# Kernel tuning notes

Hardware: AMD Instinct MI355X
Metric: run time of the kernel (lower is better)

Reference implementation:

```python
import jax, jax.numpy as jnp
from jax import lax
import numpy as np

B, R, NOBJ = 16, 64, 36
MAP = 64

def setup_inputs() -> dict:
    key = jax.random.key(0)
    ks = jax.random.split(key, 8)
    W, H = 1280, 720
    xs = jnp.sort(jax.random.uniform(ks[0], (B, NOBJ, 2), minval=0.0, maxval=float(W)), axis=-1)
    ys = jnp.sort(jax.random.uniform(ks[1], (B, NOBJ, 2), minval=0.0, maxval=float(H)), axis=-1)
    # bbox layout: [x0, y0, x1, y1] matching scale_bbox (x scaled by width, y by height)
    bboxes = jnp.stack([xs[..., 0], ys[..., 0], xs[..., 1], ys[..., 1]], axis=-1)
    obj_pairs = jax.random.randint(ks[2], (B, R, 2), 0, NOBJ, dtype=jnp.int32)
    num_rels = jnp.full((B,), R, dtype=jnp.int32)
    W1 = jax.random.normal(ks[3], (64, 2, 5, 5), jnp.float32) * 0.1
    b1 = jnp.zeros((64,), jnp.float32)
    W2 = jax.random.normal(ks[4], (32, 64, 5, 5), jnp.float32) * 0.05
    b2 = jnp.zeros((32,), jnp.float32)
    Wl = jax.random.normal(ks[5], (32, 512), jnp.float32) * 0.1
    bl = jnp.zeros((512,), jnp.float32)
    return {"bboxes": bboxes, "obj_pairs": obj_pairs, "num_rels": num_rels,
            "frame_width": W, "frame_height": H,
            "W1": W1, "b1": b1, "W2": W2, "b2": b2, "Wl": Wl, "bl": bl}

def _boxes_to_maps(boxes, frame_width, frame_height):
    # boxes: [T,4] = [x0,y0,x1,y1]; emulate scale_bbox + int() truncation + slice fill
    sfx = MAP / frame_width
    sfy = MAP / frame_height
    x0 = jnp.floor(boxes[:, 0] * sfx).astype(jnp.int32)  # col start
    x1 = jnp.floor(boxes[:, 2] * sfx).astype(jnp.int32)  # col end (exclusive)
    y0 = jnp.floor(boxes[:, 1] * sfy).astype(jnp.int32)  # row start
    y1 = jnp.floor(boxes[:, 3] * sfy).astype(jnp.int32)  # row end (exclusive)
    ix = jnp.arange(MAP)
    rows = (ix[None, :] >= y0[:, None]) & (ix[None, :] < y1[:, None])  # [T,64]
    cols = (ix[None, :] >= x0[:, None]) & (ix[None, :] < x1[:, None])  # [T,64]
    return (rows[:, :, None] & cols[:, None, :]).astype(jnp.float32)   # [T,64,64]

def _conv(x, W, b):
    y = lax.conv_general_dilated(x, W, (1, 1), 'VALID',
                                 dimension_numbers=('NCHW', 'OIHW', 'NCHW'))
    return y + b[None, :, None, None]

def _maxpool2(x):
    return lax.reduce_window(x, -jnp.inf, lax.max, (1, 1, 2, 2), (1, 1, 2, 2), 'VALID')

def reference(bboxes, obj_pairs, num_rels, frame_width, frame_height,
              W1, b1, W2, b2, Wl, bl):
    Bn = bboxes.shape[0]
    bi = jnp.arange(Bn)[:, None]
    box_a = bboxes[bi, obj_pairs[..., 0]].reshape(-1, 4)  # [T,4]
    box_b = bboxes[bi, obj_pairs[..., 1]].reshape(-1, 4)  # [T,4]
    sp = jnp.stack([_boxes_to_maps(box_a, frame_width, frame_height),
                    _boxes_to_maps(box_b, frame_width, frame_height)], axis=1)  # [T,2,64,64]
    x = _maxpool2(_conv(sp, W1, b1))        # [T,64,30,30]
    x = _maxpool2(_conv(x, W2, b2))         # [T,32,13,13]
    x = jnp.mean(x, axis=(2, 3))            # AvgPool 13x13 stride 1 -> [T,32]
    return jax.nn.relu(x @ Wl + bl)         # [T,512]
```

## Files before the change

kernel.cpp:

```cpp
#include <hip/hip_runtime.h>
#include <hip/hip_bf16.h>

#define BLOCK 1024
#define NREG  21

typedef __attribute__((ext_vector_type(8))) short short8;
typedef __attribute__((ext_vector_type(4))) float floatx4;
typedef __attribute__((ext_vector_type(4))) unsigned int uint4v;

#define SMEM_Q     0
#define SMEM_POOL  0
#define SMEM_P     72064
#define SMEM_V     72064
#define SMEM_FEAT  135568
#define SMEM_INFO  135696
#define SMEM_REP   135936
#define SMEM_TOTAL 136192

__device__ __forceinline__ int clamp05(int v) { return v < 0 ? 0 : (v > 5 ? 5 : v); }

__device__ __forceinline__ int band_id(int i, int e0, int e1, int e2, int e3) {
    int c = 0;
    #pragma unroll
    for (int k = 0; k < 5; ++k) {
        const int b0 = e0 - k, b1 = e1 - k, b2 = e2 - k, b3 = e3 - k;
        c += (b0 >= 1 && i >= b0);
        c += (b1 >= 1 && i >= b1);
        c += (b2 >= 1 && i >= b2);
        c += (b3 >= 1 && i >= b3);
    }
    return c;
}

__global__ __launch_bounds__(256) void w2_transform_kernel(
    const float* __restrict__ W2, __hip_bfloat16* __restrict__ w2t)
{
    const int idx = blockIdx.x * 256 + threadIdx.x;
    if (idx < 51200) {
        const int k   = idx & 31;
        const int n   = (idx >> 5) & 31;
        const int kc  = (idx >> 10) & 1;
        const int tap = idx >> 11;
        w2t[idx] = __float2bfloat16(W2[n*1600 + (kc*32 + k)*25 + tap]);
    }
}

__global__ __launch_bounds__(BLOCK) void vsgnet_mfma_kernel(
    const float* __restrict__ bboxes,
    const int* __restrict__ obj_pairs,
    const int* __restrict__ fw_p,
    const int* __restrict__ fh_p,
    const float* __restrict__ W1,
    const float* __restrict__ b1,
    const __hip_bfloat16* __restrict__ w2t,
    const float* __restrict__ b2,
    const float* __restrict__ Wl,
    const float* __restrict__ bl,
    float* __restrict__ out)
{
    extern __shared__ __align__(16) char smem[];
    float* Qf = (float*)(smem + SMEM_Q);
    float* Pf = (float*)(smem + SMEM_P);
    float* feat = (float*)(smem + SMEM_FEAT);
    unsigned int* rowinfo = (unsigned int*)(smem + SMEM_INFO);
    unsigned int* colinfo = rowinfo + 30;
    int* rep_row = (int*)(smem + SMEM_REP);
    int* rep_col = rep_row + 21;

    const int tid = threadIdx.x;
    const int t = blockIdx.x;
    const int bidx = t >> 6;

    const int pa = obj_pairs[2*t];
    const int pb = obj_pairs[2*t + 1];
    const float* Ab = bboxes + (bidx*36 + pa)*4;
    const float* Bb = bboxes + (bidx*36 + pb)*4;
    const float sfx = (float)(64.0 / (double)fw_p[0]);
    const float sfy = (float)(64.0 / (double)fh_p[0]);
    const int x0a = (int)floorf(Ab[0]*sfx);
    const int y0a = (int)floorf(Ab[1]*sfy);
    const int x1a = (int)floorf(Ab[2]*sfx);
    const int y1a = (int)floorf(Ab[3]*sfy);
    const int x0b = (int)floorf(Bb[0]*sfx);
    const int y0b = (int)floorf(Bb[1]*sfy);
    const int x1b = (int)floorf(Bb[2]*sfx);
    const int y1b = (int)floorf(Bb[3]*sfy);

    if (tid >= 256 && tid < 298) rep_row[tid - 256] = -1;
    if (tid < 128) {
        const int c = tid & 63;
        const int box = tid >> 6;
        const float* w = W1 + (c*2 + box)*25;
        float p[6][6];
        #pragma unroll
        for (int r = 0; r < 6; ++r) p[r][0] = 0.f;
        #pragma unroll
        for (int cc = 0; cc < 6; ++cc) p[0][cc] = 0.f;
        #pragma unroll
        for (int r = 1; r < 6; ++r)
            #pragma unroll
            for (int cc = 1; cc < 6; ++cc)
                p[r][cc] = w[(r-1)*5 + (cc-1)] + p[r-1][cc] + p[r][cc-1] - p[r-1][cc-1];
        float* Pd = Pf + (box*36)*68;
        #pragma unroll
        for (int r = 0; r < 6; ++r)
            #pragma unroll
            for (int cc = 0; cc < 6; ++cc)
                Pd[(r*6 + cc)*68 + c] = p[r][cc];
    }
    __syncthreads();

    if (tid < 30) {
        rowinfo[tid] = (unsigned)band_id(2*tid, y0a, y1a, y0b, y1b)
                     | ((unsigned)band_id(2*tid + 1, y0a, y1a, y0b, y1b) << 8);
    } else if (tid >= 32 && tid < 62) {
        const int j = tid - 32;
        colinfo[j] = (unsigned)band_id(2*j, x0a, x1a, x0b, x1b)
                   | ((unsigned)band_id(2*j + 1, x0a, x1a, x0b, x1b) << 8);
    } else if (tid >= 64 && tid < 124) {
        const int i = tid - 64;
        rep_row[band_id(i, y0a, y1a, y0b, y1b)] = i;
    } else if (tid >= 128 && tid < 188) {
        const int j = tid - 128;
        rep_col[band_id(j, x0a, x1a, x0b, x1b)] = j;
    }

    const int lane = tid & 63;
    const int wid  = tid >> 6;
    const int kg   = lane >> 4;
    const int lr   = lane & 15;

    floatx4 acc[3][2];
    #pragma unroll
    for (int s = 0; s < 3; ++s) {
        acc[s][0] = (floatx4){0.f,0.f,0.f,0.f};
        acc[s][1] = (floatx4){0.f,0.f,0.f,0.f};
    }
    int abase[3];
    #pragma unroll
    for (int s = 0; s < 3; ++s) {
        const int mt = wid + 16*s;
        int m = mt*16 + lr; if (m > 675) m = 675;
        const int pi = m / 26;
        const int pj = m - pi*26;
        abase[s] = SMEM_POOL + ((pi*30 + pj)*40 + kg*8)*2;
    }
    __syncthreads();

    for (int idx = tid; idx < 4032; idx += BLOCK) {
        const int g = idx & 15;
        const int k = idx >> 4;
        const int box = (k >= 126);
        const int kk = k - box*126;
        const int rb = kk / 6;
        const int c  = kk - rb*6;
        const int i = rep_row[rb];
        if (i >= 0) {
            int r0, r1;
            if (!box) { r0 = clamp05(y0a - i); r1 = clamp05(y1a - i); }
            else      { r0 = clamp05(y0b - i); r1 = clamp05(y1b - i); }
            const float* Pb_ = Pf + (box*36)*68 + g*4;
            const floatx4 v1 = *(const floatx4*)(Pb_ + (r1*6 + c)*68);
            const floatx4 v0 = *(const floatx4*)(Pb_ + (r0*6 + c)*68);
            *(floatx4*)(Qf + k*68 + g*4) = v1 - v0;
        }
    }
    __syncthreads();

    for (int idx = tid; idx < 3528; idx += BLOCK) {
        const int g = idx & 7;
        const int combo = idx >> 3;
        const int rb = combo / NREG;
        const int cb = combo - rb*NREG;
        const int j = rep_col[cb];
        if (j >= 0 && rep_row[rb] >= 0) {
            const int c0a = clamp05(x0a - j), c1a = clamp05(x1a - j);
            const int c0b = clamp05(x0b - j), c1b = clamp05(x1b - j);
            const float* qa = Qf + (rb*6)*68 + g*8;
            const float* qb = Qf + (126 + rb*6)*68 + g*8;
            floatx4 v0 = *(const floatx4*)(qa + c1a*68)     - *(const floatx4*)(qa + c0a*68)
                       + *(const floatx4*)(qb + c1b*68)     - *(const floatx4*)(qb + c0b*68);
            floatx4 v1 = *(const floatx4*)(qa + c1a*68 + 4) - *(const floatx4*)(qa + c0a*68 + 4)
                       + *(const floatx4*)(qb + c1b*68 + 4) - *(const floatx4*)(qb + c0b*68 + 4);
            v0 += *(const floatx4*)(b1 + g*8);
            v1 += *(const floatx4*)(b1 + g*8 + 4);
            short8 o;
            #pragma unroll
            for (int e = 0; e < 4; ++e) o[e]   = (short)__bfloat16_as_ushort(__float2bfloat16(v0[e]));
            #pragma unroll
            for (int e = 0; e < 4; ++e) o[4+e] = (short)__bfloat16_as_ushort(__float2bfloat16(v1[e]));
            *(short8*)(smem + SMEM_V + combo*144 + g*16) = o;
        }
    }
    __syncthreads();

    for (int kc = 0; kc < 2; ++kc) {
        for (int idx = tid; idx < 3600; idx += BLOCK) {
            const int g = idx & 3;
            const int cell = idx >> 2;
            const int pi = cell / 30;
            const int pj = cell - pi*30;
            const unsigned ri = rowinfo[pi], ci = colinfo[pj];
            const int rb0 = ri & 255, rb1 = (ri >> 8) & 255;
            const int cb0 = ci & 255, cb1 = (ci >> 8) & 255;
            const int voff = kc*64 + g*16;
            const uint4v u00 = *(const uint4v*)(smem + SMEM_V + (rb0*NREG + cb0)*144 + voff);
            const uint4v u01 = *(const uint4v*)(smem + SMEM_V + (rb0*NREG + cb1)*144 + voff);
            const uint4v u10 = *(const uint4v*)(smem + SMEM_V + (rb1*NREG + cb0)*144 + voff);
            const uint4v u11 = *(const uint4v*)(smem + SMEM_V + (rb1*NREG + cb1)*144 + voff);
            uint4v o;
            #pragma unroll
            for (int u = 0; u < 4; ++u) {
                const float l0 = __uint_as_float(u00[u] << 16), h0 = __uint_as_float(u00[u] & 0xffff0000u);
                const float l1 = __uint_as_float(u01[u] << 16), h1 = __uint_as_float(u01[u] & 0xffff0000u);
                const float l2 = __uint_as_float(u10[u] << 16), h2 = __uint_as_float(u10[u] & 0xffff0000u);
                const float l3 = __uint_as_float(u11[u] << 16), h3 = __uint_as_float(u11[u] & 0xffff0000u);
                const float ml = fmaxf(fmaxf(l0, l1), fmaxf(l2, l3));
                const float mh = fmaxf(fmaxf(h0, h1), fmaxf(h2, h3));
                o[u] = (__float_as_uint(ml) >> 16) | (__float_as_uint(mh) & 0xffff0000u);
            }
            *(uint4v*)(smem + SMEM_POOL + cell*80 + g*16) = o;
        }
        __syncthreads();

        {
            const __hip_bfloat16* wbk = w2t + kc*1024 + lr*32 + kg*8;
            short8 b0c = *(const short8*)(wbk);
            short8 b1c = *(const short8*)(wbk + 512);
            short8 b0n = *(const short8*)(wbk + 2048);
            short8 b1n = *(const short8*)(wbk + 2048 + 512);
            #pragma unroll
            for (int tap = 0; tap < 25; ++tap) {
                const short8 bf0 = b0c, bf1 = b1c;
                b0c = b0n; b1c = b1n;
                if (tap + 2 < 25) {
                    b0n = *(const short8*)(wbk + (tap + 2)*2048);
                    b1n = *(const short8*)(wbk + (tap + 2)*2048 + 512);
                }
                const int toffA = ((tap/5)*30 + (tap%5))*80;
                const short8 a0 = *(const short8*)(smem + abase[0] + toffA);
                const short8 a1 = *(const short8*)(smem + abase[1] + toffA);
                acc[0][0] = __builtin_amdgcn_mfma_f32_16x16x32_bf16(a0, bf0, acc[0][0], 0, 0, 0);
                acc[0][1] = __builtin_amdgcn_mfma_f32_16x16x32_bf16(a0, bf1, acc[0][1], 0, 0, 0);
                acc[1][0] = __builtin_amdgcn_mfma_f32_16x16x32_bf16(a1, bf0, acc[1][0], 0, 0, 0);
                acc[1][1] = __builtin_amdgcn_mfma_f32_16x16x32_bf16(a1, bf1, acc[1][1], 0, 0, 0);
                if (wid < 11) {
                    const short8 a2 = *(const short8*)(smem + abase[2] + toffA);
                    acc[2][0] = __builtin_amdgcn_mfma_f32_16x16x32_bf16(a2, bf0, acc[2][0], 0, 0, 0);
                    acc[2][1] = __builtin_amdgcn_mfma_f32_16x16x32_bf16(a2, bf1, acc[2][1], 0, 0, 0);
                }
            }
        }
        __syncthreads();
    }

    __hip_bfloat16* c2out = (__hip_bfloat16*)(smem + SMEM_POOL);
    if (tid < 32) feat[tid] = 0.f;
    {
        const float b2v0 = b2[lr];
        const float b2v1 = b2[16 + lr];
        #pragma unroll
        for (int s = 0; s < 3; ++s) {
            const int mt = wid + 16*s;
            if (mt < 43) {
                #pragma unroll
                for (int r = 0; r < 4; ++r) {
                    const int m = mt*16 + kg*4 + r;
                    if (m < 676) {
                        c2out[m*36 + lr]      = __float2bfloat16(acc[s][0][r] + b2v0);
                        c2out[m*36 + 16 + lr] = __float2bfloat16(acc[s][1][r] + b2v1);
                    }
                }
            }
        }
    }
    __syncthreads();

    {
        const int oc  = tid & 31;
        const int grp = tid >> 5;
        float sum = 0.f;
        for (int cell = grp; cell < 169; cell += 32) {
            const int ci = cell / 13;
            const int cj = cell - ci*13;
            const __hip_bfloat16* q = c2out + ((ci*2)*26 + cj*2)*36 + oc;
            const float v0 = __bfloat162float(q[0]);
            const float v1 = __bfloat162float(q[36]);
            const float v2 = __bfloat162float(q[936]);
            const float v3 = __bfloat162float(q[972]);
            sum += fmaxf(fmaxf(v0, v1), fmaxf(v2, v3));
        }
        atomicAdd(&feat[oc], sum * (1.0f/169.0f));
    }
    __syncthreads();

    if (tid < 512) {
        float s = bl[tid];
        #pragma unroll
        for (int ic = 0; ic < 32; ++ic)
            s = fmaf(feat[ic], Wl[ic*512 + tid], s);
        out[(size_t)t*512 + tid] = fmaxf(s, 0.f);
    }
}

extern "C" void kernel_launch(void* const* d_in, const int* in_sizes, int n_in,
                              void* d_out, int out_size, void* d_ws, size_t ws_size,
                              hipStream_t stream) {
    const float* bboxes    = (const float*)d_in[0];
    const int*   obj_pairs = (const int*)d_in[1];
    const int*   fw        = (const int*)d_in[3];
    const int*   fh        = (const int*)d_in[4];
    const float* W1        = (const float*)d_in[5];
    const float* b1        = (const float*)d_in[6];
    const float* W2        = (const float*)d_in[7];
    const float* b2        = (const float*)d_in[8];
    const float* Wl        = (const float*)d_in[9];
    const float* bl        = (const float*)d_in[10];
    float* out = (float*)d_out;
    __hip_bfloat16* w2t = (__hip_bfloat16*)d_ws;

    w2_transform_kernel<<<dim3(200), dim3(256), 0, stream>>>(W2, w2t);

    hipFuncSetAttribute((const void*)vsgnet_mfma_kernel,
                        hipFuncAttributeMaxDynamicSharedMemorySize, SMEM_TOTAL);
    vsgnet_mfma_kernel<<<dim3(1024), dim3(BLOCK), SMEM_TOTAL, stream>>>(
        bboxes, obj_pairs, fw, fh, W1, b1, w2t, b2, Wl, bl, out);
}
```

Measured before the change: 221.9 us.

## Process conv1 channels in 16-wide chunks to halve LDS footprint

Conv1 outputs are now built and pooled in four chunks of 16 channels, each computed straight from the 2D prefix sums with four-corner lookups, replacing the separate row-difference Q stage. The pooled tile and region values shrink to 16 channels, so the LDS footprint roughly halves and two 1024-thread blocks can share a CU. W2 is repacked so each MFMA K=32 step covers two taps times 16 channels, zero-padded to 13 steps per chunk. The cost is more barriers and redundant corner loads per chunk, plus non-prefetched B-fragment loads and one wasted padded tap per chunk.

```diff
diff --git a/kernel.cpp b/kernel.cpp
--- a/kernel.cpp
+++ b/kernel.cpp
@@ -8,14 +8,14 @@
 typedef __attribute__((ext_vector_type(4))) float floatx4;
 typedef __attribute__((ext_vector_type(4))) unsigned int uint4v;
 
-#define SMEM_Q     0
-#define SMEM_POOL  0
-#define SMEM_P     72064
-#define SMEM_V     72064
-#define SMEM_FEAT  135568
-#define SMEM_INFO  135696
-#define SMEM_REP   135936
-#define SMEM_TOTAL 136192
+#define SMEM_P     0
+#define SMEM_V     19584
+#define SMEM_C2    19584
+#define SMEM_POOL  37232
+#define SMEM_FEAT  73232
+#define SMEM_INFO  73360
+#define SMEM_REP   73600
+#define SMEM_TOTAL 73792
 
 __device__ __forceinline__ int clamp05(int v) { return v < 0 ? 0 : (v > 5 ? 5 : v); }
 
@@ -36,16 +36,18 @@
     const float* __restrict__ W2, __hip_bfloat16* __restrict__ w2t)
 {
     const int idx = blockIdx.x * 256 + threadIdx.x;
-    if (idx < 51200) {
-        const int k   = idx & 31;
+    if (idx < 53248) {
+        const int k32 = idx & 31;
         const int n   = (idx >> 5) & 31;
-        const int kc  = (idx >> 10) & 1;
-        const int tap = idx >> 11;
-        w2t[idx] = __float2bfloat16(W2[n*1600 + (kc*32 + k)*25 + tap]);
+        const int kt  = (idx >> 10) % 13;
+        const int c   = (idx >> 10) / 13;
+        const int tap = kt*2 + (k32 >> 4);
+        const int ic  = c*16 + (k32 & 15);
+        w2t[idx] = __float2bfloat16(tap < 25 ? W2[n*1600 + ic*25 + tap] : 0.f);
     }
 }
 
-__global__ __launch_bounds__(BLOCK) void vsgnet_mfma_kernel(
+__global__ __launch_bounds__(BLOCK, 8) void vsgnet_mfma_kernel(
     const float* __restrict__ bboxes,
     const int* __restrict__ obj_pairs,
     const int* __restrict__ fw_p,
@@ -59,7 +61,6 @@
     float* __restrict__ out)
 {
     extern __shared__ __align__(16) char smem[];
-    float* Qf = (float*)(smem + SMEM_Q);
     float* Pf = (float*)(smem + SMEM_P);
     float* feat = (float*)(smem + SMEM_FEAT);
     unsigned int* rowinfo = (unsigned int*)(smem + SMEM_INFO);
@@ -143,71 +144,59 @@
         int m = mt*16 + lr; if (m > 675) m = 675;
         const int pi = m / 26;
         const int pj = m - pi*26;
-        abase[s] = SMEM_POOL + ((pi*30 + pj)*40 + kg*8)*2;
+        abase[s] = SMEM_POOL + (pi*30 + pj)*40 + (kg & 1)*16;
     }
     __syncthreads();
 
-    for (int idx = tid; idx < 4032; idx += BLOCK) {
-        const int g = idx & 15;
-        const int k = idx >> 4;
-        const int box = (k >= 126);
-        const int kk = k - box*126;
-        const int rb = kk / 6;
-        const int c  = kk - rb*6;
-        const int i = rep_row[rb];
-        if (i >= 0) {
-            int r0, r1;
-            if (!box) { r0 = clamp05(y0a - i); r1 = clamp05(y1a - i); }
-            else      { r0 = clamp05(y0b - i); r1 = clamp05(y1b - i); }
-            const float* Pb_ = Pf + (box*36)*68 + g*4;
-            const floatx4 v1 = *(const floatx4*)(Pb_ + (r1*6 + c)*68);
-            const floatx4 v0 = *(const floatx4*)(Pb_ + (r0*6 + c)*68);
-            *(floatx4*)(Qf + k*68 + g*4) = v1 - v0;
-        }
-    }
-    __syncthreads();
-
-    for (int idx = tid; idx < 3528; idx += BLOCK) {
-        const int g = idx & 7;
-        const int combo = idx >> 3;
-        const int rb = combo / NREG;
-        const int cb = combo - rb*NREG;
-        const int j = rep_col[cb];
-        if (j >= 0 && rep_row[rb] >= 0) {
-            const int c0a = clamp05(x0a - j), c1a = clamp05(x1a - j);
-            const int c0b = clamp05(x0b - j), c1b = clamp05(x1b - j);
-            const float* qa = Qf + (rb*6)*68 + g*8;
-            const float* qb = Qf + (126 + rb*6)*68 + g*8;
-            floatx4 v0 = *(const floatx4*)(qa + c1a*68)     - *(const floatx4*)(qa + c0a*68)
-                       + *(const floatx4*)(qb + c1b*68)     - *(const floatx4*)(qb + c0b*68);
-            floatx4 v1 = *(const floatx4*)(qa + c1a*68 + 4) - *(const floatx4*)(qa + c0a*68 + 4)
-                       + *(const floatx4*)(qb + c1b*68 + 4) - *(const floatx4*)(qb + c0b*68 + 4);
-            v0 += *(const floatx4*)(b1 + g*8);
-            v1 += *(const floatx4*)(b1 + g*8 + 4);
-            short8 o;
-            #pragma unroll
-            for (int e = 0; e < 4; ++e) o[e]   = (short)__bfloat16_as_ushort(__float2bfloat16(v0[e]));
-            #pragma unroll
-            for (int e = 0; e < 4; ++e) o[4+e] = (short)__bfloat16_as_ushort(__float2bfloat16(v1[e]));
-            *(short8*)(smem + SMEM_V + combo*144 + g*16) = o;
-        }
-    }
-    __syncthreads();
-
-    for (int kc = 0; kc < 2; ++kc) {
-        for (int idx = tid; idx < 3600; idx += BLOCK) {
-            const int g = idx & 3;
-            const int cell = idx >> 2;
+    for (int c = 0; c < 4; ++c) {
+        if (tid < 882) {
+            const int g = tid & 1;
+            const int combo = tid >> 1;
+            const int rb = combo / NREG;
+            const int cb = combo - rb*NREG;
+            const int i = rep_row[rb], j = rep_col[cb];
+            if (i >= 0 && j >= 0) {
+                const int r0a_ = clamp05(y0a - i), r1a_ = clamp05(y1a - i);
+                const int r0b_ = clamp05(y0b - i), r1b_ = clamp05(y1b - i);
+                const int c0a_ = clamp05(x0a - j), c1a_ = clamp05(x1a - j);
+                const int c0b_ = clamp05(x0b - j), c1b_ = clamp05(x1b - j);
+                const float* P0 = Pf + c*16 + g*8;
+                const float* P1 = P0 + 36*68;
+                #define CORN(Pq, r_, c_, h_) (*(const floatx4*)((Pq) + ((r_)*6 + (c_))*68 + (h_)*4))
+                floatx4 vlo = CORN(P0,r1a_,c1a_,0) - CORN(P0,r0a_,c1a_,0)
+                            - CORN(P0,r1a_,c0a_,0) + CORN(P0,r0a_,c0a_,0)
+                            + CORN(P1,r1b_,c1b_,0) - CORN(P1,r0b_,c1b_,0)
+                            - CORN(P1,r1b_,c0b_,0) + CORN(P1,r0b_,c0b_,0);
+                floatx4 vhi = CORN(P0,r1a_,c1a_,1) - CORN(P0,r0a_,c1a_,1)
+                            - CORN(P0,r1a_,c0a_,1) + CORN(P0,r0a_,c0a_,1)
+                            + CORN(P1,r1b_,c1b_,1) - CORN(P1,r0b_,c1b_,1)
+                            - CORN(P1,r1b_,c0b_,1) + CORN(P1,r0b_,c0b_,1);
+                #undef CORN
+                vlo += *(const floatx4*)(b1 + c*16 + g*8);
+                vhi += *(const floatx4*)(b1 + c*16 + g*8 + 4);
+                short8 o;
+                #pragma unroll
+                for (int e = 0; e < 4; ++e) o[e]   = (short)__bfloat16_as_ushort(__float2bfloat16(vlo[e]));
+                #pragma unroll
+                for (int e = 0; e < 4; ++e) o[4+e] = (short)__bfloat16_as_ushort(__float2bfloat16(vhi[e]));
+                *(short8*)(smem + SMEM_V + combo*40 + g*16) = o;
+            }
+        }
+        __syncthreads();
+
+        for (int idx = tid; idx < 1800; idx += BLOCK) {
+            const int g = idx & 1;
+            const int cell = idx >> 1;
             const int pi = cell / 30;
             const int pj = cell - pi*30;
             const unsigned ri = rowinfo[pi], ci = colinfo[pj];
             const int rb0 = ri & 255, rb1 = (ri >> 8) & 255;
             const int cb0 = ci & 255, cb1 = (ci >> 8) & 255;
-            const int voff = kc*64 + g*16;
-            const uint4v u00 = *(const uint4v*)(smem + SMEM_V + (rb0*NREG + cb0)*144 + voff);
-            const uint4v u01 = *(const uint4v*)(smem + SMEM_V + (rb0*NREG + cb1)*144 + voff);
-            const uint4v u10 = *(const uint4v*)(smem + SMEM_V + (rb1*NREG + cb0)*144 + voff);
-            const uint4v u11 = *(const uint4v*)(smem + SMEM_V + (rb1*NREG + cb1)*144 + voff);
+            const int go = g*16;
+            const uint4v u00 = *(const uint4v*)(smem + SMEM_V + (rb0*NREG + cb0)*40 + go);
+            const uint4v u01 = *(const uint4v*)(smem + SMEM_V + (rb0*NREG + cb1)*40 + go);
+            const uint4v u10 = *(const uint4v*)(smem + SMEM_V + (rb1*NREG + cb0)*40 + go);
+            const uint4v u11 = *(const uint4v*)(smem + SMEM_V + (rb1*NREG + cb1)*40 + go);
             uint4v o;
             #pragma unroll
             for (int u = 0; u < 4; ++u) {
@@ -219,33 +208,29 @@
                 const float mh = fmaxf(fmaxf(h0, h1), fmaxf(h2, h3));
                 o[u] = (__float_as_uint(ml) >> 16) | (__float_as_uint(mh) & 0xffff0000u);
             }
-            *(uint4v*)(smem + SMEM_POOL + cell*80 + g*16) = o;
+            *(uint4v*)(smem + SMEM_POOL + cell*40 + go) = o;
         }
         __syncthreads();
 
         {
-            const __hip_bfloat16* wbk = w2t + kc*1024 + lr*32 + kg*8;
-            short8 b0c = *(const short8*)(wbk);
-            short8 b1c = *(const short8*)(wbk + 512);
-            short8 b0n = *(const short8*)(wbk + 2048);
-            short8 b1n = *(const short8*)(wbk + 2048 + 512);
+            const __hip_bfloat16* w2c = w2t + (c*13)*1024;
             #pragma unroll
-            for (int tap = 0; tap < 25; ++tap) {
-                const short8 bf0 = b0c, bf1 = b1c;
-                b0c = b0n; b1c = b1n;
-                if (tap + 2 < 25) {
-                    b0n = *(const short8*)(wbk + (tap + 2)*2048);
-                    b1n = *(const short8*)(wbk + (tap + 2)*2048 + 512);
-                }
-                const int toffA = ((tap/5)*30 + (tap%5))*80;
-                const short8 a0 = *(const short8*)(smem + abase[0] + toffA);
-                const short8 a1 = *(const short8*)(smem + abase[1] + toffA);
+            for (int kt = 0; kt < 13; ++kt) {
+                const int tap0 = 2*kt;
+                const int tap1 = (2*kt + 1 > 24) ? 24 : (2*kt + 1);
+                const int off0 = ((tap0/5)*30 + (tap0%5))*40;
+                const int off1 = ((tap1/5)*30 + (tap1%5))*40;
+                const int aoff = (kg & 2) ? off1 : off0;
+                const short8 bf0 = *(const short8*)(w2c + kt*1024 + lr*32 + kg*8);
+                const short8 bf1 = *(const short8*)(w2c + kt*1024 + (16 + lr)*32 + kg*8);
+                const short8 a0 = *(const short8*)(smem + abase[0] + aoff);
+                const short8 a1 = *(const short8*)(smem + abase[1] + aoff);
                 acc[0][0] = __builtin_amdgcn_mfma_f32_16x16x32_bf16(a0, bf0, acc[0][0], 0, 0, 0);
                 acc[0][1] = __builtin_amdgcn_mfma_f32_16x16x32_bf16(a0, bf1, acc[0][1], 0, 0, 0);
                 acc[1][0] = __builtin_amdgcn_mfma_f32_16x16x32_bf16(a1, bf0, acc[1][0], 0, 0, 0);
                 acc[1][1] = __builtin_amdgcn_mfma_f32_16x16x32_bf16(a1, bf1, acc[1][1], 0, 0, 0);
                 if (wid < 11) {
-                    const short8 a2 = *(const short8*)(smem + abase[2] + toffA);
+                    const short8 a2 = *(const short8*)(smem + abase[2] + aoff);
                     acc[2][0] = __builtin_amdgcn_mfma_f32_16x16x32_bf16(a2, bf0, acc[2][0], 0, 0, 0);
                     acc[2][1] = __builtin_amdgcn_mfma_f32_16x16x32_bf16(a2, bf1, acc[2][1], 0, 0, 0);
                 }
@@ -254,7 +239,7 @@
         __syncthreads();
     }
 
-    __hip_bfloat16* c2out = (__hip_bfloat16*)(smem + SMEM_POOL);
+    __hip_bfloat16* c2out = (__hip_bfloat16*)(smem + SMEM_C2);
     if (tid < 32) feat[tid] = 0.f;
     {
         const float b2v0 = b2[lr];
@@ -319,7 +304,7 @@
     float* out = (float*)d_out;
     __hip_bfloat16* w2t = (__hip_bfloat16*)d_ws;
 
-    w2_transform_kernel<<<dim3(200), dim3(256), 0, stream>>>(W2, w2t);
+    w2_transform_kernel<<<dim3(208), dim3(256), 0, stream>>>(W2, w2t);
 
     hipFuncSetAttribute((const void*)vsgnet_mfma_kernel,
                         hipFuncAttributeMaxDynamicSharedMemorySize, SMEM_TOTAL);
```

Measured after the change: 312.0 us. +40.6%, slower.
